# Kernel tuning notes

Measured on AMD Instinct MI355X. Metric: run time of the kernel, lower is better.

## Reference

```python
import jax, jax.numpy as jnp
import numpy as np

C_DIM = 768
NH = 12
MLP_HIDDEN = 3072


def _ln(x, g, b, eps=1e-5):
    mu = x.mean(-1, keepdims=True)
    var = ((x - mu) ** 2).mean(-1, keepdims=True)
    return (x - mu) / jnp.sqrt(var + eps) * g + b


def _mha(x, Wqkv, nh, scale):
    # x: [N, L, C]; Wqkv: [C, 3C] packed as (3, nh, hd) on output dim
    N, L, C = x.shape
    hd = C // nh
    qkv = (x @ Wqkv).reshape(N, L, 3, nh, hd)
    q, k, v = qkv[:, :, 0], qkv[:, :, 1], qkv[:, :, 2]  # [N, L, nh, hd]
    a = jnp.einsum('nqhd,nkhd->nhqk', q, k) * scale
    a = jax.nn.softmax(a, axis=-1)
    o = jnp.einsum('nhqk,nkhd->nqhd', a, v).reshape(N, L, C)
    return o


def setup_inputs() -> dict:
    key = jax.random.key(0)
    ks = jax.random.split(key, 16)
    B, T, K, C = 4, 16, 196, C_DIM
    s = 0.02
    inp = {
        'x': jax.random.normal(ks[0], (B, 1 + K * T, C), jnp.float32),
        'B': B, 'T': T, 'K': K,
        'ln1_g': jnp.ones((C,)), 'ln1_b': jnp.zeros((C,)),
        'lnt_g': jnp.ones((C,)), 'lnt_b': jnp.zeros((C,)),
        'ln2_g': jnp.ones((C,)), 'ln2_b': jnp.zeros((C,)),
        'lncls_g': jnp.ones((C,)), 'lncls_b': jnp.zeros((C,)),
        'Wqkv_s': jax.random.normal(ks[1], (C, 3 * C)) * s,
        'Wproj_s': jax.random.normal(ks[2], (C, C)) * s,
        'bproj_s': jnp.zeros((C,)),
        'Wqkv4': jax.random.normal(ks[3], (C, 3 * C)) * s,
        'Wqkv8': jax.random.normal(ks[4], (C, 3 * C)) * s,
        'Wqkv16': jax.random.normal(ks[5], (C, 3 * C)) * s,
        'Wp4': jax.random.normal(ks[6], (C, C)) * s, 'bp4': jnp.zeros((C,)),
        'Wp8': jax.random.normal(ks[7], (C, C)) * s, 'bp8': jnp.zeros((C,)),
        'Wp16': jax.random.normal(ks[8], (C, C)) * s, 'bp16': jnp.zeros((C,)),
        'Wtfc': jax.random.normal(ks[9], (C, C)) * s, 'btfc': jnp.zeros((C,)),
        'Wfc1': jax.random.normal(ks[10], (C, MLP_HIDDEN)) * s, 'bfc1': jnp.zeros((MLP_HIDDEN,)),
        'Wfc2': jax.random.normal(ks[11], (MLP_HIDDEN, C)) * s, 'bfc2': jnp.zeros((C,)),
    }
    return inp


def reference(x, B, T, K, ln1_g, ln1_b, lnt_g, lnt_b, ln2_g, ln2_b,
              lncls_g, lncls_b, Wqkv_s, Wproj_s, bproj_s,
              Wqkv4, Wqkv8, Wqkv16, Wp4, bp4, Wp8, bp8, Wp16, bp16,
              Wtfc, btfc, Wfc1, bfc1, Wfc2, bfc2):
    C = x.shape[-1]
    nh = NH
    scale = (C // nh) ** -0.5
    t1, t2 = T // 4, T // 2

    # ---- multi-scale temporal attention (eval mode: all dropout identity) ----
    xt = x[:, 1:, :].reshape(B, K, T, C).reshape(B * K, T, C)
    xt_n = _ln(xt, lnt_g, lnt_b)
    x4 = _mha(xt_n[:, T - t1:], Wqkv4, nh, scale) @ Wp4 + bp4    # [BK, t1, C]
    x8 = _mha(xt_n[:, t2:], Wqkv8, nh, scale) @ Wp8 + bp8        # [BK, t2, C]
    x16 = _mha(xt_n, Wqkv16, nh, scale) @ Wp16 + bp16            # [BK, T, C]
    # windowed fusion of overlapping scales
    x8 = jnp.concatenate([x8[:, :t1], 0.5 * x8[:, t1:] + 0.5 * x4], axis=1)
    x16 = jnp.concatenate([x16[:, :t2], 0.5 * x16[:, t2:] + 0.5 * x8], axis=1)
    res_temp = x16.reshape(B, K * T, C)
    xt_full = res_temp @ Wtfc + btfc + x[:, 1:, :]               # [B, K*T, C]

    # ---- spatial attention with replicated CLS token ----
    init_cls = x[:, 0:1, :]                                      # [B, 1, C]
    cls_rep = jnp.broadcast_to(init_cls, (B, T, C)).reshape(B * T, 1, C)
    xs = xt_full.reshape(B, K, T, C).transpose(0, 2, 1, 3).reshape(B * T, K, C)
    xs = jnp.concatenate([cls_rep, xs], axis=1)                  # [B*T, K+1, C]
    res_spatial = _mha(_ln(xs, ln1_g, ln1_b), Wqkv_s, nh, scale) @ Wproj_s + bproj_s

    # ---- CLS aggregation over time ----
    cls_sp = _ln(res_spatial[:, 0, :].reshape(B, T, C), lncls_g, lncls_b)
    target = cls_sp[:, -1:, :]                                   # [B, 1, C]
    attn2 = jax.nn.softmax(jnp.einsum('bqc,btc->bqt', target, cls_sp), axis=-1)
    cls_sp = attn2 @ cls_sp                                      # [B, 1, C]

    x_s = res_spatial[:, 1:, :].reshape(B, T, K, C).transpose(0, 2, 1, 3).reshape(B, K * T, C)
    x_cat = jnp.concatenate([init_cls, xt_full], axis=1) + jnp.concatenate([cls_sp, x_s], axis=1)

    # ---- MLP residual ----
    h = _ln(x_cat, ln2_g, ln2_b)
    h = jax.nn.gelu(h @ Wfc1 + bfc1, approximate=False) @ Wfc2 + bfc2
    return x_cat + h
```

## Files before the change

### kernel.cpp

```cpp
#include <hip/hip_runtime.h>
#include <hip/hip_bf16.h>
#include <stdint.h>

#define BF16 __hip_bfloat16

typedef __attribute__((ext_vector_type(8))) short short8;
typedef __attribute__((ext_vector_type(2))) short short2v;
typedef __attribute__((ext_vector_type(4))) float floatx4;

typedef const __attribute__((address_space(1))) void* gas_cvp;
typedef __attribute__((address_space(3))) void* las_vp;

__device__ __forceinline__ float bf2f(BF16 v) { return __bfloat162float(v); }
__device__ __forceinline__ BF16 f2bf(float v) { return __float2bfloat16(v); }

__global__ __launch_bounds__(256) void wtrans(const float* __restrict__ W,
                                              BF16* __restrict__ Wt, int K, int N) {
    __shared__ float t[32][33];
    int k0 = blockIdx.x * 32, n0 = blockIdx.y * 32;
    int tx = threadIdx.x & 31, ty = threadIdx.x >> 5;
#pragma unroll
    for (int i = 0; i < 32; i += 8) t[ty + i][tx] = W[(size_t)(k0 + ty + i) * N + n0 + tx];
    __syncthreads();
#pragma unroll
    for (int i = 0; i < 32; i += 8)
        Wt[(size_t)(n0 + ty + i) * K + k0 + tx] = f2bf(t[tx][ty + i]);
}

template <int MODE>
__global__ __launch_bounds__(256) void ln_kernel(const float* __restrict__ src0,
                                                 const float* __restrict__ src1,
                                                 const BF16* __restrict__ srcb,
                                                 const float* __restrict__ g,
                                                 const float* __restrict__ bta,
                                                 BF16* __restrict__ dst_bf,
                                                 float* __restrict__ dst_f) {
    const int r = blockIdx.x, tid = threadIdx.x;
    float x0, x1, x2;
    if (MODE == 3) {
        const BF16* src = srcb + (size_t)r * 197 * 768;
        x0 = bf2f(src[tid]); x1 = bf2f(src[tid + 256]); x2 = bf2f(src[tid + 512]);
    } else {
        const float* src;
        if (MODE == 0) {
            int b = r / 3136, rr = r - b * 3136;
            src = src0 + ((size_t)b * 3137 + 1 + rr) * 768;
        } else if (MODE == 1) {
            int bt = r / 197, j = r - bt * 197;
            int b = bt >> 4, t = bt & 15;
            if (j == 0) src = src0 + (size_t)b * 3137 * 768;
            else        src = src1 + ((size_t)(b * 3137 + 1) + (size_t)(j - 1) * 16 + t) * 768;
        } else {
            src = src0 + (size_t)r * 768;
        }
        x0 = src[tid]; x1 = src[tid + 256]; x2 = src[tid + 512];
    }
    float s = x0 + x1 + x2;
    float ss = x0 * x0 + x1 * x1 + x2 * x2;
    __shared__ float red[8];
#pragma unroll
    for (int o = 32; o > 0; o >>= 1) { s += __shfl_down(s, o); ss += __shfl_down(ss, o); }
    if ((tid & 63) == 0) { red[tid >> 6] = s; red[4 + (tid >> 6)] = ss; }
    __syncthreads();
    s = red[0] + red[1] + red[2] + red[3];
    ss = red[4] + red[5] + red[6] + red[7];
    const float mu = s * (1.0f / 768.0f);
    const float var = ss * (1.0f / 768.0f) - mu * mu;
    const float rstd = rsqrtf(var + 1e-5f);
#pragma unroll
    for (int i = 0; i < 3; ++i) {
        int c = tid + i * 256;
        float xv = (i == 0) ? x0 : (i == 1) ? x1 : x2;
        float y = (xv - mu) * rstd * g[c] + bta[c];
        if (MODE == 3) dst_f[(size_t)r * 768 + c] = y;
        else           dst_bf[(size_t)r * 768 + c] = f2bf(y);
    }
}

template <int AMAP, int OMODE>
__global__ __launch_bounds__(256) void gemm_bf16(const BF16* __restrict__ A,
                                                 const BF16* __restrict__ Bt,
                                                 const float* __restrict__ bias,
                                                 const void* res,
                                                 void* Cout,
                                                 int M, int N, int K) {
    __shared__ BF16 Al[128 * 64];
    __shared__ BF16 Bl[128 * 64];
    const int tid = threadIdx.x;
    const int lane = tid & 63;
    const int w = tid >> 6;

    const int gx = gridDim.x;
    const int nwg = gx * (int)gridDim.y;
    const int orig = (int)blockIdx.y * gx + (int)blockIdx.x;
    const int xcd = orig & 7;
    const int idx = orig >> 3;
    const int q8 = nwg >> 3, r8 = nwg & 7;
    const int wgid = (xcd < r8 ? xcd * (q8 + 1) : r8 * (q8 + 1) + (xcd - r8) * q8) + idx;
    const int bn0 = (wgid % gx) * 128;
    const int bm0 = (wgid / gx) * 128;

    const BF16* gsrc[8];
    BF16* ldst[8];
    const int rin = lane >> 3;
    const int kblk = (lane & 7) ^ rin;
#pragma unroll
    for (int j = 0; j < 8; ++j) {
        int c = w * 8 + j;
        if (c < 16) {
            int gr = bm0 + c * 8 + rin;
            if (gr > M - 1) gr = M - 1;
            if (AMAP == 1) gr = (gr >> 3) * 16 + 8 + (gr & 7);
            if (AMAP == 2) gr = (gr >> 2) * 16 + 12 + (gr & 3);
            gsrc[j] = A + (size_t)gr * K + kblk * 8;
            ldst[j] = Al + c * 512;
        } else {
            int gn = bn0 + (c - 16) * 8 + rin;
            gsrc[j] = Bt + (size_t)gn * K + kblk * 8;
            ldst[j] = Bl + (c - 16) * 512;
        }
    }

    const int wm = (w & 1) * 64;
    const int wn = (w >> 1) * 64;
    const int fr = lane & 15;
    const int fq = lane >> 4;
    const int sw = fr & 7;
    const int o0 = (fq ^ sw) * 8;
    const int o1 = ((fq + 4) ^ sw) * 8;
    const BF16* pa[4];
    const BF16* pb[4];
#pragma unroll
    for (int t = 0; t < 4; ++t) {
        pa[t] = Al + (wm + t * 16 + fr) * 64;
        pb[t] = Bl + (wn + t * 16 + fr) * 64;
    }

    floatx4 acc[4][4];
#pragma unroll
    for (int i = 0; i < 4; ++i)
#pragma unroll
        for (int j = 0; j < 4; ++j) acc[i][j] = (floatx4){0.f, 0.f, 0.f, 0.f};

    for (int k0 = 0; k0 < K; k0 += 64) {
#pragma unroll
        for (int j = 0; j < 8; ++j) {
            __builtin_amdgcn_global_load_lds((gas_cvp)gsrc[j], (las_vp)ldst[j], 16, 0, 0);
            gsrc[j] += 64;
        }
        __syncthreads();
        {
            short8 af[4], bfr[4];
#pragma unroll
            for (int t = 0; t < 4; ++t) {
                af[t] = *(const short8*)(pa[t] + o0);
                bfr[t] = *(const short8*)(pb[t] + o0);
            }
#pragma unroll
            for (int mt = 0; mt < 4; ++mt)
#pragma unroll
                for (int nt = 0; nt < 4; ++nt)
                    acc[mt][nt] = __builtin_amdgcn_mfma_f32_16x16x32_bf16(af[mt], bfr[nt], acc[mt][nt], 0, 0, 0);
#pragma unroll
            for (int t = 0; t < 4; ++t) {
                af[t] = *(const short8*)(pa[t] + o1);
                bfr[t] = *(const short8*)(pb[t] + o1);
            }
#pragma unroll
            for (int mt = 0; mt < 4; ++mt)
#pragma unroll
                for (int nt = 0; nt < 4; ++nt)
                    acc[mt][nt] = __builtin_amdgcn_mfma_f32_16x16x32_bf16(af[mt], bfr[nt], acc[mt][nt], 0, 0, 0);
        }
        __syncthreads();
    }

#pragma unroll
    for (int mt = 0; mt < 4; ++mt) {
#pragma unroll
        for (int nt = 0; nt < 4; ++nt) {
            const int gcol = bn0 + wn + nt * 16 + fr;
#pragma unroll
            for (int r = 0; r < 4; ++r) {
                const int grow = bm0 + wm + mt * 16 + fq * 4 + r;
                if (grow < M) {
                    float v = acc[mt][nt][r];
                    if (OMODE != 0 && OMODE != 8) v += bias[gcol];
                    if (OMODE == 0 || OMODE == 1) {
                        ((BF16*)Cout)[(size_t)grow * N + gcol] = f2bf(v);
                    } else if (OMODE == 2) {
                        int t8 = grow & 7;
                        int rr = (grow >> 3) * 16 + 8 + t8;
                        float w8 = (t8 < 4) ? 0.5f : 0.25f;
                        BF16* R = (BF16*)Cout;
                        size_t o = (size_t)rr * 768 + gcol;
                        R[o] = f2bf(0.5f * bf2f(R[o]) + w8 * v);
                    } else if (OMODE == 3) {
                        int t4 = grow & 3;
                        int rr = (grow >> 2) * 16 + 12 + t4;
                        BF16* R = (BF16*)Cout;
                        size_t o = (size_t)rr * 768 + gcol;
                        R[o] = f2bf(bf2f(R[o]) + 0.25f * v);
                    } else if (OMODE == 4) {
                        int b = grow / 3136;
                        size_t xrow = (size_t)b * 3137 + 1 + (grow - b * 3136);
                        ((float*)Cout)[xrow * 768 + gcol] =
                            v + ((const float*)res)[xrow * 768 + gcol];
                    } else if (OMODE == 6) {
                        float u = v * (0.7978845608f + 0.0356774081f * v * v);
                        v = v / (1.0f + __expf(-2.0f * u));
                        ((BF16*)Cout)[(size_t)grow * N + gcol] = f2bf(v);
                    } else {
                        v += ((const float*)res)[(size_t)grow * N + gcol];
                        ((float*)Cout)[(size_t)grow * N + gcol] = v;
                    }
                }
            }
        }
    }
}

template <int L, int NT>
__global__ __launch_bounds__(NT) void temporal_attn(const BF16* __restrict__ qkv,
                                                    BF16* __restrict__ outp) {
    __shared__ float q[L * 64];
    __shared__ float k[L * 65];
    __shared__ float v[L * 64];
    __shared__ float S[L * L];
    const int bh = blockIdx.x;
    const int b = bh / 12, h = bh % 12;
    const int tid = threadIdx.x;
    const size_t rb = (size_t)b * L;
    for (int idx = tid; idx < L * 64; idx += NT) {
        int i = idx >> 6, d = idx & 63;
        size_t base = (rb + i) * 2304 + h * 64 + d;
        q[i * 64 + d] = bf2f(qkv[base]);
        k[i * 65 + d] = bf2f(qkv[base + 768]);
        v[i * 64 + d] = bf2f(qkv[base + 1536]);
    }
    __syncthreads();
    for (int idx = tid; idx < L * L; idx += NT) {
        int i = idx / L, j = idx % L;
        float a = 0.f;
#pragma unroll
        for (int d = 0; d < 64; ++d) a += q[i * 64 + d] * k[j * 65 + d];
        S[idx] = a * 0.125f;
    }
    __syncthreads();
    if (tid < L) {
        float mx = -1e30f;
        for (int j = 0; j < L; ++j) mx = fmaxf(mx, S[tid * L + j]);
        float sm = 0.f;
        for (int j = 0; j < L; ++j) { float e = __expf(S[tid * L + j] - mx); S[tid * L + j] = e; sm += e; }
        float inv = 1.0f / sm;
        for (int j = 0; j < L; ++j) S[tid * L + j] *= inv;
    }
    __syncthreads();
    for (int idx = tid; idx < L * 64; idx += NT) {
        int i = idx >> 6, d = idx & 63;
        float acc = 0.f;
#pragma unroll
        for (int j = 0; j < L; ++j) acc += S[i * L + j] * v[j * 64 + d];
        outp[(rb + i) * 768 + h * 64 + d] = f2bf(acc);
    }
}

__global__ __launch_bounds__(256) void spatial_attn_mfma(const BF16* __restrict__ qkv,
                                                         BF16* __restrict__ outp) {
    const int bid = blockIdx.x;
    const int qt = bid & 3;
    const int h = (bid >> 2) % 12;
    const int bt = bid / 48;
    const int rowbase = bt * 197;
    __shared__ BF16 Ks[208 * 72];
    __shared__ BF16 Vt[64 * 232];
    __shared__ BF16 Pl[4][16 * 232];
    const int tid = threadIdx.x;
    const int lane = tid & 63;
    const int w = tid >> 6;
    const int ln = lane & 15;
    const int quad = lane >> 4;

    for (int it = tid; it < 208 * 8; it += 256) {
        int key = it >> 3, c = it & 7;
        int kc = key < 197 ? key : 196;
        short8 gk = *(const short8*)(qkv + (size_t)(rowbase + kc) * 2304 + 768 + h * 64 + c * 8);
        *(short8*)&Ks[key * 72 + c * 8] = gk;
    }
    for (int it = tid; it < 112 * 8; it += 256) {
        int p = it >> 3, c = it & 7;
        int kc0 = (2 * p < 197) ? 2 * p : 196;
        int kc1 = (2 * p + 1 < 197) ? 2 * p + 1 : 196;
        short8 a = *(const short8*)(qkv + (size_t)(rowbase + kc0) * 2304 + 1536 + h * 64 + c * 8);
        short8 b = *(const short8*)(qkv + (size_t)(rowbase + kc1) * 2304 + 1536 + h * 64 + c * 8);
#pragma unroll
        for (int e = 0; e < 8; ++e) {
            short2v pr;
            pr[0] = a[e];
            pr[1] = b[e];
            *(short2v*)&Vt[(c * 8 + e) * 232 + 2 * p] = pr;
        }
    }
    __syncthreads();

    const int m0 = qt * 64 + w * 16;
    int qrow = m0 + ln; if (qrow > 196) qrow = 196;
    const BF16* qptr = qkv + (size_t)(rowbase + qrow) * 2304 + h * 64 + quad * 8;
    short8 aq0 = *(const short8*)(qptr);
    short8 aq1 = *(const short8*)(qptr + 32);

    floatx4 sacc[13];
#pragma unroll
    for (int nt = 0; nt < 13; ++nt) sacc[nt] = (floatx4){0.f, 0.f, 0.f, 0.f};
#pragma unroll
    for (int nt = 0; nt < 13; ++nt) {
        const BF16* kb = &Ks[(nt * 16 + ln) * 72 + quad * 8];
        short8 b0 = *(const short8*)kb;
        short8 b1 = *(const short8*)(kb + 32);
        sacc[nt] = __builtin_amdgcn_mfma_f32_16x16x32_bf16(aq0, b0, sacc[nt], 0, 0, 0);
        sacc[nt] = __builtin_amdgcn_mfma_f32_16x16x32_bf16(aq1, b1, sacc[nt], 0, 0, 0);
    }

#pragma unroll
    for (int r = 0; r < 4; ++r) {
        float mx = -1e30f;
#pragma unroll
        for (int nt = 0; nt < 13; ++nt) {
            float s = sacc[nt][r] * 0.125f;
            sacc[nt][r] = s;
            if (nt * 16 + ln < 197) mx = fmaxf(mx, s);
        }
        mx = fmaxf(mx, __shfl_xor(mx, 1));
        mx = fmaxf(mx, __shfl_xor(mx, 2));
        mx = fmaxf(mx, __shfl_xor(mx, 4));
        mx = fmaxf(mx, __shfl_xor(mx, 8));
        float sum = 0.f;
#pragma unroll
        for (int nt = 0; nt < 13; ++nt) {
            float e = (nt * 16 + ln < 197) ? __expf(sacc[nt][r] - mx) : 0.f;
            sacc[nt][r] = e;
            sum += e;
        }
        sum += __shfl_xor(sum, 1);
        sum += __shfl_xor(sum, 2);
        sum += __shfl_xor(sum, 4);
        sum += __shfl_xor(sum, 8);
        float inv = 1.0f / sum;
#pragma unroll
        for (int nt = 0; nt < 13; ++nt) sacc[nt][r] *= inv;
    }

    BF16* pw = Pl[w];
#pragma unroll
    for (int nt = 0; nt < 13; ++nt)
#pragma unroll
        for (int r = 0; r < 4; ++r)
            pw[(quad * 4 + r) * 232 + nt * 16 + ln] = f2bf(sacc[nt][r]);
#pragma unroll
    for (int r = 0; r < 4; ++r)
        pw[(quad * 4 + r) * 232 + 208 + ln] = f2bf(0.f);

    floatx4 oacc[4];
#pragma unroll
    for (int nt = 0; nt < 4; ++nt) oacc[nt] = (floatx4){0.f, 0.f, 0.f, 0.f};
    for (int kb = 0; kb < 7; ++kb) {
        short8 ap = *(const short8*)&pw[ln * 232 + kb * 32 + quad * 8];
#pragma unroll
        for (int nt = 0; nt < 4; ++nt) {
            short8 bv = *(const short8*)&Vt[(nt * 16 + ln) * 232 + kb * 32 + quad * 8];
            oacc[nt] = __builtin_amdgcn_mfma_f32_16x16x32_bf16(ap, bv, oacc[nt], 0, 0, 0);
        }
    }

#pragma unroll
    for (int nt = 0; nt < 4; ++nt) {
        int dim = nt * 16 + ln;
#pragma unroll
        for (int r = 0; r < 4; ++r) {
            int q = m0 + quad * 4 + r;
            if (q < 197)
                outp[(size_t)(rowbase + q) * 768 + h * 64 + dim] = f2bf(oacc[nt][r]);
        }
    }
}

__global__ __launch_bounds__(256) void cls_attn_kernel(const float* __restrict__ clsln,
                                                       float* __restrict__ clsout) {
    const int b = blockIdx.x;
    const int tid = threadIdx.x;
    __shared__ float dots[16];
    __shared__ float aw[16];
    const int t = tid >> 4, l16 = tid & 15;
    const float* tgt = clsln + (size_t)(b * 16 + 15) * 768;
    const float* row = clsln + (size_t)(b * 16 + t) * 768;
    float p = 0.f;
    for (int c = l16; c < 768; c += 16) p += tgt[c] * row[c];
#pragma unroll
    for (int o = 8; o > 0; o >>= 1) p += __shfl_down(p, o, 16);
    if (l16 == 0) dots[t] = p;
    __syncthreads();
    if (tid == 0) {
        float mx = -1e30f;
        for (int j = 0; j < 16; ++j) mx = fmaxf(mx, dots[j]);
        float s = 0.f;
        for (int j = 0; j < 16; ++j) { aw[j] = __expf(dots[j] - mx); s += aw[j]; }
        float inv = 1.0f / s;
        for (int j = 0; j < 16; ++j) aw[j] *= inv;
    }
    __syncthreads();
    for (int c = tid; c < 768; c += 256) {
        float acc = 0.f;
#pragma unroll
        for (int j = 0; j < 16; ++j) acc += aw[j] * clsln[(size_t)(b * 16 + j) * 768 + c];
        clsout[(size_t)b * 768 + c] = acc;
    }
}

__global__ __launch_bounds__(256) void xcat_kernel(const float* __restrict__ x,
                                                   const BF16* __restrict__ res_sp,
                                                   const float* __restrict__ clsout,
                                                   float* outbuf) {
    const int gidx = blockIdx.x;
    const int b = gidx / 3137, j = gidx - b * 3137;
    const int tid = threadIdx.x;
    if (j == 0) {
        const float* xr = x + (size_t)b * 3137 * 768;
        const float* cr = clsout + (size_t)b * 768;
#pragma unroll
        for (int i = 0; i < 3; ++i) {
            int c = tid + i * 256;
            outbuf[(size_t)gidx * 768 + c] = xr[c] + cr[c];
        }
    } else {
        const int p = j - 1, k = p >> 4, t = p & 15;
        const BF16* rs = res_sp + (size_t)((b * 16 + t) * 197 + 1 + k) * 768;
#pragma unroll
        for (int i = 0; i < 3; ++i) {
            int c = tid + i * 256;
            outbuf[(size_t)gidx * 768 + c] = outbuf[(size_t)gidx * 768 + c] + bf2f(rs[c]);
        }
    }
}

extern "C" void kernel_launch(void* const* d_in, const int* in_sizes, int n_in,
                              void* d_out, int out_size, void* d_ws, size_t ws_size,
                              hipStream_t stream) {
    const float* x       = (const float*)d_in[0];
    const float* ln1_g   = (const float*)d_in[4];
    const float* ln1_b   = (const float*)d_in[5];
    const float* lnt_g   = (const float*)d_in[6];
    const float* lnt_b   = (const float*)d_in[7];
    const float* ln2_g   = (const float*)d_in[8];
    const float* ln2_b   = (const float*)d_in[9];
    const float* lncls_g = (const float*)d_in[10];
    const float* lncls_b = (const float*)d_in[11];
    const float* Wqkv_s  = (const float*)d_in[12];
    const float* Wproj_s = (const float*)d_in[13];
    const float* bproj_s = (const float*)d_in[14];
    const float* Wqkv4   = (const float*)d_in[15];
    const float* Wqkv8   = (const float*)d_in[16];
    const float* Wqkv16  = (const float*)d_in[17];
    const float* Wp4     = (const float*)d_in[18];
    const float* bp4     = (const float*)d_in[19];
    const float* Wp8     = (const float*)d_in[20];
    const float* bp8     = (const float*)d_in[21];
    const float* Wp16    = (const float*)d_in[22];
    const float* bp16    = (const float*)d_in[23];
    const float* Wtfc    = (const float*)d_in[24];
    const float* btfc    = (const float*)d_in[25];
    const float* Wfc1    = (const float*)d_in[26];
    const float* bfc1    = (const float*)d_in[27];
    const float* Wfc2    = (const float*)d_in[28];
    const float* bfc2    = (const float*)d_in[29];
    float* out = (float*)d_out;

    const size_t oW0 = 0;
    const size_t oW1 = 4718592;
    const size_t oR1 = 9437184;
    const size_t oR2 = 28803072;
    const size_t oR3 = 48070656;
    const size_t oR4 = 77119488;
    const size_t oCL = 96485376;
    const size_t oCO = 96681984;
    const size_t NEED = 96694272;
    if (ws_size < NEED) return;
    char* ws = (char*)d_ws;

    BF16* w0       = (BF16*)(ws + oW0);
    BF16* w1       = (BF16*)(ws + oW1);
    BF16* xtn      = (BF16*)(ws + oR1);
    BF16* atts     = (BF16*)(ws + oR1);
    BF16* hln      = (BF16*)(ws + oR1);
    BF16* res_temp = (BF16*)(ws + oR2);
    BF16* h1       = (BF16*)(ws + oR2);
    BF16* qkv      = (BF16*)(ws + oR3);
    BF16* att      = (BF16*)(ws + oR4);
    BF16* xsn      = (BF16*)(ws + oR4);
    BF16* res_sp   = (BF16*)(ws + oR4);
    float* clsln   = (float*)(ws + oCL);
    float* clsout  = (float*)(ws + oCO);

    ln_kernel<0><<<12544, 256, 0, stream>>>(x, nullptr, nullptr, lnt_g, lnt_b, xtn, nullptr);

    wtrans<<<dim3(24, 72), 256, 0, stream>>>(Wqkv16, w0, 768, 2304);
    for (int c = 0; c < 2; ++c) {
        gemm_bf16<0, 0><<<dim3(18, 49), 256, 0, stream>>>(xtn + (size_t)c * 6272 * 768, w0, nullptr, nullptr, qkv, 6272, 2304, 768);
        temporal_attn<16, 256><<<4704, 256, 0, stream>>>(qkv, att + (size_t)c * 6272 * 768);
    }
    wtrans<<<dim3(24, 24), 256, 0, stream>>>(Wp16, w1, 768, 768);
    gemm_bf16<0, 1><<<dim3(6, 98), 256, 0, stream>>>(att, w1, bp16, nullptr, res_temp, 12544, 768, 768);

    wtrans<<<dim3(24, 72), 256, 0, stream>>>(Wqkv8, w0, 768, 2304);
    gemm_bf16<1, 0><<<dim3(18, 49), 256, 0, stream>>>(xtn, w0, nullptr, nullptr, qkv, 6272, 2304, 768);
    temporal_attn<8, 64><<<9408, 64, 0, stream>>>(qkv, att);
    wtrans<<<dim3(24, 24), 256, 0, stream>>>(Wp8, w1, 768, 768);
    gemm_bf16<0, 2><<<dim3(6, 49), 256, 0, stream>>>(att, w1, bp8, nullptr, res_temp, 6272, 768, 768);

    wtrans<<<dim3(24, 72), 256, 0, stream>>>(Wqkv4, w0, 768, 2304);
    gemm_bf16<2, 0><<<dim3(18, 25), 256, 0, stream>>>(xtn, w0, nullptr, nullptr, qkv, 3136, 2304, 768);
    temporal_attn<4, 64><<<9408, 64, 0, stream>>>(qkv, att);
    wtrans<<<dim3(24, 24), 256, 0, stream>>>(Wp4, w1, 768, 768);
    gemm_bf16<0, 3><<<dim3(6, 25), 256, 0, stream>>>(att, w1, bp4, nullptr, res_temp, 3136, 768, 768);

    wtrans<<<dim3(24, 24), 256, 0, stream>>>(Wtfc, w0, 768, 768);
    gemm_bf16<0, 4><<<dim3(6, 98), 256, 0, stream>>>(res_temp, w0, btfc, x, out, 12544, 768, 768);

    ln_kernel<1><<<12608, 256, 0, stream>>>(x, out, nullptr, ln1_g, ln1_b, xsn, nullptr);
    wtrans<<<dim3(24, 72), 256, 0, stream>>>(Wqkv_s, w1, 768, 2304);
    for (int c = 0; c < 2; ++c) {
        gemm_bf16<0, 0><<<dim3(18, 50), 256, 0, stream>>>(xsn + (size_t)c * 6304 * 768, w1, nullptr, nullptr, qkv, 6304, 2304, 768);
        spatial_attn_mfma<<<1536, 256, 0, stream>>>(qkv, atts + (size_t)c * 6304 * 768);
    }
    wtrans<<<dim3(24, 24), 256, 0, stream>>>(Wproj_s, w0, 768, 768);
    gemm_bf16<0, 1><<<dim3(6, 99), 256, 0, stream>>>(atts, w0, bproj_s, nullptr, res_sp, 12608, 768, 768);

    ln_kernel<3><<<64, 256, 0, stream>>>(nullptr, nullptr, res_sp, lncls_g, lncls_b, nullptr, clsln);
    cls_attn_kernel<<<4, 256, 0, stream>>>(clsln, clsout);

    xcat_kernel<<<12548, 256, 0, stream>>>(x, res_sp, clsout, out);
    ln_kernel<2><<<12548, 256, 0, stream>>>(out, nullptr, nullptr, ln2_g, ln2_b, hln, nullptr);

    wtrans<<<dim3(24, 96), 256, 0, stream>>>(Wfc1, w0, 768, 3072);
    wtrans<<<dim3(48, 24), 256, 0, stream>>>(Wfc2, w1, 1536, 768);
    wtrans<<<dim3(48, 24), 256, 0, stream>>>(Wfc2 + (size_t)1536 * 768, w1 + (size_t)768 * 1536, 1536, 768);

    gemm_bf16<0, 6><<<dim3(12, 99), 256, 0, stream>>>(hln, w0, bfc1, nullptr, h1, 12548, 1536, 768);
    gemm_bf16<0, 7><<<dim3(6, 99), 256, 0, stream>>>(h1, w1, bfc2, out, out, 12548, 768, 1536);
    gemm_bf16<0, 6><<<dim3(12, 99), 256, 0, stream>>>(hln, w0 + (size_t)1536 * 768, bfc1 + 1536, nullptr, h1, 12548, 1536, 768);
    gemm_bf16<0, 8><<<dim3(6, 99), 256, 0, stream>>>(h1, w1 + (size_t)768 * 1536, nullptr, out, out, 12548, 768, 1536);
}
```

Before: 1.034 ms.

## Add 256x256-tile 512-thread GEMM with XCD remapping and swap in for most GEMMs

Adds a new bf16 MFMA GEMM kernel that uses 256x256 output tiles with 8 waves, double-buffered LDS filled by direct global-to-LDS loads with a swizzled layout, and a workgroup-id remap that groups tiles by XCD. Most GEMM launches move to this kernel, with grids shrunk to match. The larger tiles are meant to raise data reuse and MFMA density and cut per-tile overhead. In exchange, register and LDS pressure rise, and fewer workgroups (e.g. 3x49 or 9x13) can leave CUs idle and waste work on tail-tile padding.

```diff
diff --git a/kernel.cpp b/kernel.cpp
--- a/kernel.cpp
+++ b/kernel.cpp
@@ -220,6 +220,165 @@
     }
 }
 
+template <int AMAP, int OMODE>
+__global__ __launch_bounds__(512, 2) void gemm256(const BF16* __restrict__ A,
+                                                  const BF16* __restrict__ Bt,
+                                                  const float* __restrict__ bias,
+                                                  const void* res,
+                                                  void* Cout,
+                                                  int M, int N, int K) {
+    __shared__ BF16 Als[2][256 * 64];
+    __shared__ BF16 Bls[2][256 * 64];
+    const int tid = threadIdx.x;
+    const int lane = tid & 63;
+    const int w = tid >> 6;
+    const int wm = w >> 2, wn = w & 3;
+
+    const int gx = gridDim.x;
+    const int nwg = gx * (int)gridDim.y;
+    const int orig = (int)blockIdx.y * gx + (int)blockIdx.x;
+    const int xcd = orig & 7, sidx = orig >> 3;
+    const int q8 = nwg >> 3, r8 = nwg & 7;
+    const int wgid = (xcd < r8 ? xcd * (q8 + 1) : r8 * (q8 + 1) + (xcd - r8) * q8) + sidx;
+    const int bn0 = (wgid % gx) * 256;
+    const int bm0 = (wgid / gx) * 256;
+
+    const char* gsrc[8];
+#pragma unroll
+    for (int j = 0; j < 8; ++j) {
+        const int L = (j & 3) * 8192 + w * 1024 + lane * 16;
+        const int row = L >> 7;
+        const int cb = (L & 127) ^ (((L >> 9) & 1) << 5);
+        if (j < 4) {
+            int gr = bm0 + row;
+            if (gr > M - 1) gr = M - 1;
+            if (AMAP == 1) gr = (gr >> 3) * 16 + 8 + (gr & 7);
+            if (AMAP == 2) gr = (gr >> 2) * 16 + 12 + (gr & 3);
+            gsrc[j] = (const char*)A + (size_t)gr * (size_t)(K * 2) + cb;
+        } else {
+            gsrc[j] = (const char*)Bt + (size_t)(bn0 + row) * (size_t)(K * 2) + cb;
+        }
+    }
+
+    const int fr = lane & 15, fq = lane >> 4;
+    const int s5 = ((fr >> 2) & 1) << 5;
+    const int cx = (fq * 16) ^ s5;
+    const int aRow = (wm * 128 + fr) * 128;
+    const int bRow = (wn * 64 + fr) * 128;
+
+    floatx4 acc[8][4];
+#pragma unroll
+    for (int i = 0; i < 8; ++i)
+#pragma unroll
+        for (int j = 0; j < 4; ++j) acc[i][j] = (floatx4){0.f, 0.f, 0.f, 0.f};
+
+#pragma unroll
+    for (int j = 0; j < 8; ++j) {
+        char* dst = (char*)(j < 4 ? Als[0] : Bls[0]) + (j & 3) * 8192 + w * 1024;
+        __builtin_amdgcn_global_load_lds((gas_cvp)gsrc[j], (las_vp)dst, 16, 0, 0);
+        gsrc[j] += 128;
+    }
+    asm volatile("s_waitcnt vmcnt(0)" ::: "memory");
+    asm volatile("s_barrier" ::: "memory");
+
+#define LDA8(mt, kk) (*(const short8*)(Ab + aRow + (mt) * 2048 + (kk) * 64 + cx))
+#define LDB8(nt, kk) (*(const short8*)(Bb + bRow + (nt) * 2048 + (kk) * 64 + cx))
+#define STG(j, dstbuf) do {                                                        \
+        __builtin_amdgcn_global_load_lds((gas_cvp)gsrc[j],                         \
+            (las_vp)((dstbuf) + ((j) & 3) * 8192 + w * 1024), 16, 0, 0);           \
+        gsrc[j] += 128; } while (0)
+#define MFMA16(MB) do {                                                            \
+        _Pragma("unroll")                                                          \
+        for (int mtl = 0; mtl < 4; ++mtl) {                                        \
+            _Pragma("unroll")                                                      \
+            for (int ntl = 0; ntl < 4; ++ntl)                                      \
+                acc[(MB) * 4 + mtl][ntl] = __builtin_amdgcn_mfma_f32_16x16x32_bf16( \
+                    afr[mtl], bfr[ntl], acc[(MB) * 4 + mtl][ntl], 0, 0, 0);        \
+        } } while (0)
+
+    const int NT = K >> 6;
+    for (int kt = 0; kt < NT; ++kt) {
+        const char* Ab = (const char*)Als[kt & 1];
+        const char* Bb = (const char*)Bls[kt & 1];
+        char* An = (char*)Als[(kt + 1) & 1];
+        char* Bn = (char*)Bls[(kt + 1) & 1];
+        const bool pf = (kt + 1 < NT);
+        short8 afr[4], bfr[4];
+
+        bfr[0] = LDB8(0, 0); bfr[1] = LDB8(1, 0); bfr[2] = LDB8(2, 0); bfr[3] = LDB8(3, 0);
+        afr[0] = LDA8(0, 0); afr[1] = LDA8(1, 0); afr[2] = LDA8(2, 0); afr[3] = LDA8(3, 0);
+        if (pf) { STG(0, An); STG(1, An); STG(2, An); STG(3, An); }
+        asm volatile("s_barrier" ::: "memory");
+        __builtin_amdgcn_s_setprio(1);
+        MFMA16(0);
+        __builtin_amdgcn_s_setprio(0);
+        __builtin_amdgcn_sched_barrier(0);
+        asm volatile("s_barrier" ::: "memory");
+
+        afr[0] = LDA8(4, 0); afr[1] = LDA8(5, 0); afr[2] = LDA8(6, 0); afr[3] = LDA8(7, 0);
+        if (pf) { STG(4, Bn); STG(5, Bn); STG(6, Bn); STG(7, Bn); }
+        asm volatile("s_barrier" ::: "memory");
+        __builtin_amdgcn_s_setprio(1);
+        MFMA16(1);
+        __builtin_amdgcn_s_setprio(0);
+        __builtin_amdgcn_sched_barrier(0);
+        asm volatile("s_barrier" ::: "memory");
+
+        bfr[0] = LDB8(0, 1); bfr[1] = LDB8(1, 1); bfr[2] = LDB8(2, 1); bfr[3] = LDB8(3, 1);
+        afr[0] = LDA8(0, 1); afr[1] = LDA8(1, 1); afr[2] = LDA8(2, 1); afr[3] = LDA8(3, 1);
+        asm volatile("s_barrier" ::: "memory");
+        __builtin_amdgcn_s_setprio(1);
+        MFMA16(0);
+        __builtin_amdgcn_s_setprio(0);
+        __builtin_amdgcn_sched_barrier(0);
+        asm volatile("s_barrier" ::: "memory");
+
+        afr[0] = LDA8(4, 1); afr[1] = LDA8(5, 1); afr[2] = LDA8(6, 1); afr[3] = LDA8(7, 1);
+        asm volatile("s_barrier" ::: "memory");
+        __builtin_amdgcn_s_setprio(1);
+        MFMA16(1);
+        __builtin_amdgcn_s_setprio(0);
+        __builtin_amdgcn_sched_barrier(0);
+        asm volatile("s_waitcnt vmcnt(0)" ::: "memory");
+        asm volatile("s_barrier" ::: "memory");
+    }
+#undef LDA8
+#undef LDB8
+#undef STG
+#undef MFMA16
+
+#pragma unroll
+    for (int mt = 0; mt < 8; ++mt) {
+#pragma unroll
+        for (int nt = 0; nt < 4; ++nt) {
+            const int gcol = bn0 + wn * 64 + nt * 16 + fr;
+#pragma unroll
+            for (int r = 0; r < 4; ++r) {
+                const int grow = bm0 + wm * 128 + mt * 16 + fq * 4 + r;
+                if (grow < M) {
+                    float v = acc[mt][nt][r];
+                    if (OMODE != 0 && OMODE != 8) v += bias[gcol];
+                    if (OMODE == 0 || OMODE == 1) {
+                        ((BF16*)Cout)[(size_t)grow * N + gcol] = f2bf(v);
+                    } else if (OMODE == 4) {
+                        int b = grow / 3136;
+                        size_t xrow = (size_t)b * 3137 + 1 + (grow - b * 3136);
+                        ((float*)Cout)[xrow * 768 + gcol] =
+                            v + ((const float*)res)[xrow * 768 + gcol];
+                    } else if (OMODE == 6) {
+                        float u = v * (0.7978845608f + 0.0356774081f * v * v);
+                        v = v / (1.0f + __expf(-2.0f * u));
+                        ((BF16*)Cout)[(size_t)grow * N + gcol] = f2bf(v);
+                    } else {
+                        v += ((const float*)res)[(size_t)grow * N + gcol];
+                        ((float*)Cout)[(size_t)grow * N + gcol] = v;
+                    }
+                }
+            }
+        }
+    }
+}
+
 template <int L, int NT>
 __global__ __launch_bounds__(NT) void temporal_attn(const BF16* __restrict__ qkv,
                                                     BF16* __restrict__ outp) {
@@ -504,35 +663,35 @@
 
     wtrans<<<dim3(24, 72), 256, 0, stream>>>(Wqkv16, w0, 768, 2304);
     for (int c = 0; c < 2; ++c) {
-        gemm_bf16<0, 0><<<dim3(18, 49), 256, 0, stream>>>(xtn + (size_t)c * 6272 * 768, w0, nullptr, nullptr, qkv, 6272, 2304, 768);
+        gemm256<0, 0><<<dim3(9, 25), 512, 0, stream>>>(xtn + (size_t)c * 6272 * 768, w0, nullptr, nullptr, qkv, 6272, 2304, 768);
         temporal_attn<16, 256><<<4704, 256, 0, stream>>>(qkv, att + (size_t)c * 6272 * 768);
     }
     wtrans<<<dim3(24, 24), 256, 0, stream>>>(Wp16, w1, 768, 768);
-    gemm_bf16<0, 1><<<dim3(6, 98), 256, 0, stream>>>(att, w1, bp16, nullptr, res_temp, 12544, 768, 768);
+    gemm256<0, 1><<<dim3(3, 49), 512, 0, stream>>>(att, w1, bp16, nullptr, res_temp, 12544, 768, 768);
 
     wtrans<<<dim3(24, 72), 256, 0, stream>>>(Wqkv8, w0, 768, 2304);
-    gemm_bf16<1, 0><<<dim3(18, 49), 256, 0, stream>>>(xtn, w0, nullptr, nullptr, qkv, 6272, 2304, 768);
+    gemm256<1, 0><<<dim3(9, 25), 512, 0, stream>>>(xtn, w0, nullptr, nullptr, qkv, 6272, 2304, 768);
     temporal_attn<8, 64><<<9408, 64, 0, stream>>>(qkv, att);
     wtrans<<<dim3(24, 24), 256, 0, stream>>>(Wp8, w1, 768, 768);
     gemm_bf16<0, 2><<<dim3(6, 49), 256, 0, stream>>>(att, w1, bp8, nullptr, res_temp, 6272, 768, 768);
 
     wtrans<<<dim3(24, 72), 256, 0, stream>>>(Wqkv4, w0, 768, 2304);
-    gemm_bf16<2, 0><<<dim3(18, 25), 256, 0, stream>>>(xtn, w0, nullptr, nullptr, qkv, 3136, 2304, 768);
+    gemm256<2, 0><<<dim3(9, 13), 512, 0, stream>>>(xtn, w0, nullptr, nullptr, qkv, 3136, 2304, 768);
     temporal_attn<4, 64><<<9408, 64, 0, stream>>>(qkv, att);
     wtrans<<<dim3(24, 24), 256, 0, stream>>>(Wp4, w1, 768, 768);
     gemm_bf16<0, 3><<<dim3(6, 25), 256, 0, stream>>>(att, w1, bp4, nullptr, res_temp, 3136, 768, 768);
 
     wtrans<<<dim3(24, 24), 256, 0, stream>>>(Wtfc, w0, 768, 768);
-    gemm_bf16<0, 4><<<dim3(6, 98), 256, 0, stream>>>(res_temp, w0, btfc, x, out, 12544, 768, 768);
+    gemm256<0, 4><<<dim3(3, 49), 512, 0, stream>>>(res_temp, w0, btfc, x, out, 12544, 768, 768);
 
     ln_kernel<1><<<12608, 256, 0, stream>>>(x, out, nullptr, ln1_g, ln1_b, xsn, nullptr);
     wtrans<<<dim3(24, 72), 256, 0, stream>>>(Wqkv_s, w1, 768, 2304);
     for (int c = 0; c < 2; ++c) {
-        gemm_bf16<0, 0><<<dim3(18, 50), 256, 0, stream>>>(xsn + (size_t)c * 6304 * 768, w1, nullptr, nullptr, qkv, 6304, 2304, 768);
+        gemm256<0, 0><<<dim3(9, 25), 512, 0, stream>>>(xsn + (size_t)c * 6304 * 768, w1, nullptr, nullptr, qkv, 6304, 2304, 768);
         spatial_attn_mfma<<<1536, 256, 0, stream>>>(qkv, atts + (size_t)c * 6304 * 768);
     }
     wtrans<<<dim3(24, 24), 256, 0, stream>>>(Wproj_s, w0, 768, 768);
-    gemm_bf16<0, 1><<<dim3(6, 99), 256, 0, stream>>>(atts, w0, bproj_s, nullptr, res_sp, 12608, 768, 768);
+    gemm256<0, 1><<<dim3(3, 50), 512, 0, stream>>>(atts, w0, bproj_s, nullptr, res_sp, 12608, 768, 768);
 
     ln_kernel<3><<<64, 256, 0, stream>>>(nullptr, nullptr, res_sp, lncls_g, lncls_b, nullptr, clsln);
     cls_attn_kernel<<<4, 256, 0, stream>>>(clsln, clsout);
@@ -544,8 +703,8 @@
     wtrans<<<dim3(48, 24), 256, 0, stream>>>(Wfc2, w1, 1536, 768);
     wtrans<<<dim3(48, 24), 256, 0, stream>>>(Wfc2 + (size_t)1536 * 768, w1 + (size_t)768 * 1536, 1536, 768);
 
-    gemm_bf16<0, 6><<<dim3(12, 99), 256, 0, stream>>>(hln, w0, bfc1, nullptr, h1, 12548, 1536, 768);
-    gemm_bf16<0, 7><<<dim3(6, 99), 256, 0, stream>>>(h1, w1, bfc2, out, out, 12548, 768, 1536);
-    gemm_bf16<0, 6><<<dim3(12, 99), 256, 0, stream>>>(hln, w0 + (size_t)1536 * 768, bfc1 + 1536, nullptr, h1, 12548, 1536, 768);
-    gemm_bf16<0, 8><<<dim3(6, 99), 256, 0, stream>>>(h1, w1 + (size_t)768 * 1536, nullptr, out, out, 12548, 768, 1536);
-}
+    gemm256<0, 6><<<dim3(6, 50), 512, 0, stream>>>(hln, w0, bfc1, nullptr, h1, 12548, 1536, 768);
+    gemm256<0, 7><<<dim3(3, 50), 512, 0, stream>>>(h1, w1, bfc2, out, out, 12548, 768, 1536);
+    gemm256<0, 6><<<dim3(6, 50), 512, 0, stream>>>(hln, w0 + (size_t)1536 * 768, bfc1 + 1536, nullptr, h1, 12548, 1536, 768);
+    gemm256<0, 8><<<dim3(3, 50), 512, 0, stream>>>(h1, w1 + (size_t)768 * 1536, nullptr, out, out, 12548, 768, 1536);
+}
```

After: 1.184 ms. 1.14x slower.

## Add triple-buffered 256x128 ring GEMM with direct-to-LDS loads and XCD remap

Applied to the files above, without the earlier changes.

Adds a new GEMM kernel with 512 threads and 256x128 output tiles. It uses a three-stage LDS ring filled by global_load_lds with swizzled addressing, manual vmcnt waits, and an XCD-aware workgroup remapping. Most GEMM launches switch to it, with grids halved along M. The aim is to overlap global loads with MFMA work and improve operand reuse and L2 locality, at the cost of about 144KB of LDS per block and fewer blocks for the smaller GEMMs.

```diff
diff --git a/kernel.cpp b/kernel.cpp
--- a/kernel.cpp
+++ b/kernel.cpp
@@ -220,6 +220,172 @@
     }
 }
 
+template <int AMAP, int OMODE>
+__global__ __launch_bounds__(512, 2) void gemm_ring(const BF16* __restrict__ A,
+                                                    const BF16* __restrict__ Bt,
+                                                    const float* __restrict__ bias,
+                                                    const void* res,
+                                                    void* Cout,
+                                                    int M, int N, int K) {
+    __shared__ BF16 ring[3][24576];
+    const int tid = threadIdx.x;
+    const int lane = tid & 63;
+    const int w = tid >> 6;
+    const int wm = w >> 1, wn = w & 1;
+
+    const int gx = gridDim.x;
+    const int nwg = gx * (int)gridDim.y;
+    const int orig = (int)blockIdx.y * gx + (int)blockIdx.x;
+    const int xcd = orig & 7, sidx = orig >> 3;
+    const int q8 = nwg >> 3, r8 = nwg & 7;
+    const int wgid = (xcd < r8 ? xcd * (q8 + 1) : r8 * (q8 + 1) + (xcd - r8) * q8) + sidx;
+    const int bn0 = (wgid % gx) * 128;
+    const int bm0 = (wgid / gx) * 256;
+
+    const char* gsrc[6];
+    int lofs[6];
+#pragma unroll
+    for (int j = 0; j < 6; ++j) {
+        const int base = (j < 4) ? j * 8192 : 32768 + (j - 4) * 8192;
+        const int L = base + w * 1024 + lane * 16;
+        lofs[j] = L;
+        const int rl = (j < 4) ? (L >> 7) : ((L - 32768) >> 7);
+        const int cb = (L & 127) ^ ((rl & 7) << 4);
+        if (j < 4) {
+            int gr = bm0 + rl;
+            if (gr > M - 1) gr = M - 1;
+            if (AMAP == 1) gr = (gr >> 3) * 16 + 8 + (gr & 7);
+            if (AMAP == 2) gr = (gr >> 2) * 16 + 12 + (gr & 3);
+            gsrc[j] = (const char*)A + (size_t)gr * (size_t)(K * 2) + cb;
+        } else {
+            gsrc[j] = (const char*)Bt + (size_t)(bn0 + rl) * (size_t)(K * 2) + cb;
+        }
+    }
+
+    const int fr = lane & 15, fq = lane >> 4;
+    const int xm = (fr & 7) << 4;
+    const int cx0 = (fq * 16) ^ xm;
+    const int cx1 = (fq * 16 + 64) ^ xm;
+    const int aOff = (wm * 64 + fr) * 128;
+    const int bOff = 32768 + (wn * 64 + fr) * 128;
+
+    floatx4 acc[4][4];
+#pragma unroll
+    for (int i = 0; i < 4; ++i)
+#pragma unroll
+        for (int j = 0; j < 4; ++j) acc[i][j] = (floatx4){0.f, 0.f, 0.f, 0.f};
+
+    char* const ringbase = (char*)&ring[0][0];
+
+#pragma unroll
+    for (int p = 0; p < 2; ++p) {
+#pragma unroll
+        for (int j = 0; j < 6; ++j) {
+            __builtin_amdgcn_global_load_lds((gas_cvp)gsrc[j],
+                                             (las_vp)(ringbase + p * 49152 + lofs[j]), 16, 0, 0);
+            gsrc[j] += 128;
+        }
+    }
+
+#define LDA8(mt, kk) (*(const short8*)(Ab + aOff + (mt) * 2048 + ((kk) ? cx1 : cx0)))
+#define LDB8(nt, kk) (*(const short8*)(Ab + bOff + (nt) * 2048 + ((kk) ? cx1 : cx0)))
+
+    const int NT = K >> 6;
+    int cur = 0, sb = 2;
+    for (int t = 0; t < NT; ++t) {
+        if (t < NT - 1) asm volatile("s_waitcnt vmcnt(6)" ::: "memory");
+        else            asm volatile("s_waitcnt vmcnt(0)" ::: "memory");
+        asm volatile("s_barrier" ::: "memory");
+        if (t + 2 < NT) {
+            char* dst = ringbase + sb * 49152;
+#pragma unroll
+            for (int j = 0; j < 6; ++j) {
+                __builtin_amdgcn_global_load_lds((gas_cvp)gsrc[j], (las_vp)(dst + lofs[j]), 16, 0, 0);
+                gsrc[j] += 128;
+            }
+        }
+        const char* Ab = ringbase + cur * 49152;
+        {
+            short8 a0, a1, a2, a3, b0, b1, b2, b3;
+            b0 = LDB8(0, 0); b1 = LDB8(1, 0); b2 = LDB8(2, 0); b3 = LDB8(3, 0);
+            a0 = LDA8(0, 0); a1 = LDA8(1, 0); a2 = LDA8(2, 0); a3 = LDA8(3, 0);
+            __builtin_amdgcn_s_setprio(1);
+            acc[0][0] = __builtin_amdgcn_mfma_f32_16x16x32_bf16(a0, b0, acc[0][0], 0, 0, 0);
+            acc[0][1] = __builtin_amdgcn_mfma_f32_16x16x32_bf16(a0, b1, acc[0][1], 0, 0, 0);
+            acc[0][2] = __builtin_amdgcn_mfma_f32_16x16x32_bf16(a0, b2, acc[0][2], 0, 0, 0);
+            acc[0][3] = __builtin_amdgcn_mfma_f32_16x16x32_bf16(a0, b3, acc[0][3], 0, 0, 0);
+            acc[1][0] = __builtin_amdgcn_mfma_f32_16x16x32_bf16(a1, b0, acc[1][0], 0, 0, 0);
+            acc[1][1] = __builtin_amdgcn_mfma_f32_16x16x32_bf16(a1, b1, acc[1][1], 0, 0, 0);
+            acc[1][2] = __builtin_amdgcn_mfma_f32_16x16x32_bf16(a1, b2, acc[1][2], 0, 0, 0);
+            acc[1][3] = __builtin_amdgcn_mfma_f32_16x16x32_bf16(a1, b3, acc[1][3], 0, 0, 0);
+            acc[2][0] = __builtin_amdgcn_mfma_f32_16x16x32_bf16(a2, b0, acc[2][0], 0, 0, 0);
+            acc[2][1] = __builtin_amdgcn_mfma_f32_16x16x32_bf16(a2, b1, acc[2][1], 0, 0, 0);
+            acc[2][2] = __builtin_amdgcn_mfma_f32_16x16x32_bf16(a2, b2, acc[2][2], 0, 0, 0);
+            acc[2][3] = __builtin_amdgcn_mfma_f32_16x16x32_bf16(a2, b3, acc[2][3], 0, 0, 0);
+            acc[3][0] = __builtin_amdgcn_mfma_f32_16x16x32_bf16(a3, b0, acc[3][0], 0, 0, 0);
+            acc[3][1] = __builtin_amdgcn_mfma_f32_16x16x32_bf16(a3, b1, acc[3][1], 0, 0, 0);
+            acc[3][2] = __builtin_amdgcn_mfma_f32_16x16x32_bf16(a3, b2, acc[3][2], 0, 0, 0);
+            acc[3][3] = __builtin_amdgcn_mfma_f32_16x16x32_bf16(a3, b3, acc[3][3], 0, 0, 0);
+            __builtin_amdgcn_s_setprio(0);
+            b0 = LDB8(0, 1); b1 = LDB8(1, 1); b2 = LDB8(2, 1); b3 = LDB8(3, 1);
+            a0 = LDA8(0, 1); a1 = LDA8(1, 1); a2 = LDA8(2, 1); a3 = LDA8(3, 1);
+            __builtin_amdgcn_s_setprio(1);
+            acc[0][0] = __builtin_amdgcn_mfma_f32_16x16x32_bf16(a0, b0, acc[0][0], 0, 0, 0);
+            acc[0][1] = __builtin_amdgcn_mfma_f32_16x16x32_bf16(a0, b1, acc[0][1], 0, 0, 0);
+            acc[0][2] = __builtin_amdgcn_mfma_f32_16x16x32_bf16(a0, b2, acc[0][2], 0, 0, 0);
+            acc[0][3] = __builtin_amdgcn_mfma_f32_16x16x32_bf16(a0, b3, acc[0][3], 0, 0, 0);
+            acc[1][0] = __builtin_amdgcn_mfma_f32_16x16x32_bf16(a1, b0, acc[1][0], 0, 0, 0);
+            acc[1][1] = __builtin_amdgcn_mfma_f32_16x16x32_bf16(a1, b1, acc[1][1], 0, 0, 0);
+            acc[1][2] = __builtin_amdgcn_mfma_f32_16x16x32_bf16(a1, b2, acc[1][2], 0, 0, 0);
+            acc[1][3] = __builtin_amdgcn_mfma_f32_16x16x32_bf16(a1, b3, acc[1][3], 0, 0, 0);
+            acc[2][0] = __builtin_amdgcn_mfma_f32_16x16x32_bf16(a2, b0, acc[2][0], 0, 0, 0);
+            acc[2][1] = __builtin_amdgcn_mfma_f32_16x16x32_bf16(a2, b1, acc[2][1], 0, 0, 0);
+            acc[2][2] = __builtin_amdgcn_mfma_f32_16x16x32_bf16(a2, b2, acc[2][2], 0, 0, 0);
+            acc[2][3] = __builtin_amdgcn_mfma_f32_16x16x32_bf16(a2, b3, acc[2][3], 0, 0, 0);
+            acc[3][0] = __builtin_amdgcn_mfma_f32_16x16x32_bf16(a3, b0, acc[3][0], 0, 0, 0);
+            acc[3][1] = __builtin_amdgcn_mfma_f32_16x16x32_bf16(a3, b1, acc[3][1], 0, 0, 0);
+            acc[3][2] = __builtin_amdgcn_mfma_f32_16x16x32_bf16(a3, b2, acc[3][2], 0, 0, 0);
+            acc[3][3] = __builtin_amdgcn_mfma_f32_16x16x32_bf16(a3, b3, acc[3][3], 0, 0, 0);
+            __builtin_amdgcn_s_setprio(0);
+        }
+        cur = (cur == 2) ? 0 : cur + 1;
+        sb  = (sb == 2) ? 0 : sb + 1;
+    }
+#undef LDA8
+#undef LDB8
+
+#pragma unroll
+    for (int mt = 0; mt < 4; ++mt) {
+#pragma unroll
+        for (int nt = 0; nt < 4; ++nt) {
+            const int gcol = bn0 + wn * 64 + nt * 16 + fr;
+#pragma unroll
+            for (int r = 0; r < 4; ++r) {
+                const int grow = bm0 + wm * 64 + mt * 16 + fq * 4 + r;
+                if (grow < M) {
+                    float v = acc[mt][nt][r];
+                    if (OMODE != 0 && OMODE != 8) v += bias[gcol];
+                    if (OMODE == 0 || OMODE == 1) {
+                        ((BF16*)Cout)[(size_t)grow * N + gcol] = f2bf(v);
+                    } else if (OMODE == 4) {
+                        int b = grow / 3136;
+                        size_t xrow = (size_t)b * 3137 + 1 + (grow - b * 3136);
+                        ((float*)Cout)[xrow * 768 + gcol] =
+                            v + ((const float*)res)[xrow * 768 + gcol];
+                    } else if (OMODE == 6) {
+                        float u = v * (0.7978845608f + 0.0356774081f * v * v);
+                        v = v / (1.0f + __expf(-2.0f * u));
+                        ((BF16*)Cout)[(size_t)grow * N + gcol] = f2bf(v);
+                    } else {
+                        v += ((const float*)res)[(size_t)grow * N + gcol];
+                        ((float*)Cout)[(size_t)grow * N + gcol] = v;
+                    }
+                }
+            }
+        }
+    }
+}
+
 template <int L, int NT>
 __global__ __launch_bounds__(NT) void temporal_attn(const BF16* __restrict__ qkv,
                                                     BF16* __restrict__ outp) {
@@ -504,35 +670,35 @@
 
     wtrans<<<dim3(24, 72), 256, 0, stream>>>(Wqkv16, w0, 768, 2304);
     for (int c = 0; c < 2; ++c) {
-        gemm_bf16<0, 0><<<dim3(18, 49), 256, 0, stream>>>(xtn + (size_t)c * 6272 * 768, w0, nullptr, nullptr, qkv, 6272, 2304, 768);
+        gemm_ring<0, 0><<<dim3(18, 25), 512, 0, stream>>>(xtn + (size_t)c * 6272 * 768, w0, nullptr, nullptr, qkv, 6272, 2304, 768);
         temporal_attn<16, 256><<<4704, 256, 0, stream>>>(qkv, att + (size_t)c * 6272 * 768);
     }
     wtrans<<<dim3(24, 24), 256, 0, stream>>>(Wp16, w1, 768, 768);
-    gemm_bf16<0, 1><<<dim3(6, 98), 256, 0, stream>>>(att, w1, bp16, nullptr, res_temp, 12544, 768, 768);
+    gemm_ring<0, 1><<<dim3(6, 49), 512, 0, stream>>>(att, w1, bp16, nullptr, res_temp, 12544, 768, 768);
 
     wtrans<<<dim3(24, 72), 256, 0, stream>>>(Wqkv8, w0, 768, 2304);
-    gemm_bf16<1, 0><<<dim3(18, 49), 256, 0, stream>>>(xtn, w0, nullptr, nullptr, qkv, 6272, 2304, 768);
+    gemm_ring<1, 0><<<dim3(18, 25), 512, 0, stream>>>(xtn, w0, nullptr, nullptr, qkv, 6272, 2304, 768);
     temporal_attn<8, 64><<<9408, 64, 0, stream>>>(qkv, att);
     wtrans<<<dim3(24, 24), 256, 0, stream>>>(Wp8, w1, 768, 768);
     gemm_bf16<0, 2><<<dim3(6, 49), 256, 0, stream>>>(att, w1, bp8, nullptr, res_temp, 6272, 768, 768);
 
     wtrans<<<dim3(24, 72), 256, 0, stream>>>(Wqkv4, w0, 768, 2304);
-    gemm_bf16<2, 0><<<dim3(18, 25), 256, 0, stream>>>(xtn, w0, nullptr, nullptr, qkv, 3136, 2304, 768);
+    gemm_ring<2, 0><<<dim3(18, 13), 512, 0, stream>>>(xtn, w0, nullptr, nullptr, qkv, 3136, 2304, 768);
     temporal_attn<4, 64><<<9408, 64, 0, stream>>>(qkv, att);
     wtrans<<<dim3(24, 24), 256, 0, stream>>>(Wp4, w1, 768, 768);
     gemm_bf16<0, 3><<<dim3(6, 25), 256, 0, stream>>>(att, w1, bp4, nullptr, res_temp, 3136, 768, 768);
 
     wtrans<<<dim3(24, 24), 256, 0, stream>>>(Wtfc, w0, 768, 768);
-    gemm_bf16<0, 4><<<dim3(6, 98), 256, 0, stream>>>(res_temp, w0, btfc, x, out, 12544, 768, 768);
+    gemm_ring<0, 4><<<dim3(6, 49), 512, 0, stream>>>(res_temp, w0, btfc, x, out, 12544, 768, 768);
 
     ln_kernel<1><<<12608, 256, 0, stream>>>(x, out, nullptr, ln1_g, ln1_b, xsn, nullptr);
     wtrans<<<dim3(24, 72), 256, 0, stream>>>(Wqkv_s, w1, 768, 2304);
     for (int c = 0; c < 2; ++c) {
-        gemm_bf16<0, 0><<<dim3(18, 50), 256, 0, stream>>>(xsn + (size_t)c * 6304 * 768, w1, nullptr, nullptr, qkv, 6304, 2304, 768);
+        gemm_ring<0, 0><<<dim3(18, 25), 512, 0, stream>>>(xsn + (size_t)c * 6304 * 768, w1, nullptr, nullptr, qkv, 6304, 2304, 768);
         spatial_attn_mfma<<<1536, 256, 0, stream>>>(qkv, atts + (size_t)c * 6304 * 768);
     }
     wtrans<<<dim3(24, 24), 256, 0, stream>>>(Wproj_s, w0, 768, 768);
-    gemm_bf16<0, 1><<<dim3(6, 99), 256, 0, stream>>>(atts, w0, bproj_s, nullptr, res_sp, 12608, 768, 768);
+    gemm_ring<0, 1><<<dim3(6, 50), 512, 0, stream>>>(atts, w0, bproj_s, nullptr, res_sp, 12608, 768, 768);
 
     ln_kernel<3><<<64, 256, 0, stream>>>(nullptr, nullptr, res_sp, lncls_g, lncls_b, nullptr, clsln);
     cls_attn_kernel<<<4, 256, 0, stream>>>(clsln, clsout);
@@ -544,8 +710,8 @@
     wtrans<<<dim3(48, 24), 256, 0, stream>>>(Wfc2, w1, 1536, 768);
     wtrans<<<dim3(48, 24), 256, 0, stream>>>(Wfc2 + (size_t)1536 * 768, w1 + (size_t)768 * 1536, 1536, 768);
 
-    gemm_bf16<0, 6><<<dim3(12, 99), 256, 0, stream>>>(hln, w0, bfc1, nullptr, h1, 12548, 1536, 768);
-    gemm_bf16<0, 7><<<dim3(6, 99), 256, 0, stream>>>(h1, w1, bfc2, out, out, 12548, 768, 1536);
-    gemm_bf16<0, 6><<<dim3(12, 99), 256, 0, stream>>>(hln, w0 + (size_t)1536 * 768, bfc1 + 1536, nullptr, h1, 12548, 1536, 768);
-    gemm_bf16<0, 8><<<dim3(6, 99), 256, 0, stream>>>(h1, w1 + (size_t)768 * 1536, nullptr, out, out, 12548, 768, 1536);
-}
+    gemm_ring<0, 6><<<dim3(12, 50), 512, 0, stream>>>(hln, w0, bfc1, nullptr, h1, 12548, 1536, 768);
+    gemm_ring<0, 7><<<dim3(6, 50), 512, 0, stream>>>(h1, w1, bfc2, out, out, 12548, 768, 1536);
+    gemm_ring<0, 6><<<dim3(12, 50), 512, 0, stream>>>(hln, w0 + (size_t)1536 * 768, bfc1 + 1536, nullptr, h1, 12548, 1536, 768);
+    gemm_ring<0, 8><<<dim3(6, 50), 512, 0, stream>>>(h1, w1 + (size_t)768 * 1536, nullptr, out, out, 12548, 768, 1536);
+}
```

Measured after the change: 1.253 ms. 21.1% more time.
